# Kernel tuning notes

Hardware: AMD Instinct MI355X
Metric: run time of the kernel (lower is better)

Reference implementation:

```python
import jax, jax.numpy as jnp
import numpy as np

HIDDEN = 1024
NUM_HEADS = 16
HEAD_DIM = HIDDEN // NUM_HEADS


def setup_inputs() -> dict:
    key = jax.random.key(0)
    k1, k2, k3, k4, k5 = jax.random.split(key, 5)
    B, S, T, H = 2, 2048, 2048, HIDDEN
    scale = 0.02
    return {
        "query": jax.random.normal(k1, (B, S, H), dtype=jnp.float32),
        "key_value": jax.random.normal(k2, (B, T, H), dtype=jnp.float32),
        "Wq": jax.random.normal(k3, (H, H), dtype=jnp.float32) * scale,
        "Wkv": jax.random.normal(k4, (H, 2 * H), dtype=jnp.float32) * scale,
        "Wc": jax.random.normal(k5, (H, H), dtype=jnp.float32) * scale,
    }


def reference(query, key_value, Wq, Wkv, Wc):
    B, S, H = query.shape
    T = key_value.shape[1]
    nh, hd = NUM_HEADS, HEAD_DIM

    q = query @ Wq                                  # [B,S,H]
    kv = key_value @ Wkv                            # [B,T,2H]
    k, v = kv[..., :H], kv[..., H:]

    # [B, nh, S|T, hd]
    q = q.reshape(B, S, nh, hd).transpose(0, 2, 1, 3)
    k = k.reshape(B, T, nh, hd).transpose(0, 2, 1, 3)
    v = v.reshape(B, T, nh, hd).transpose(0, 2, 1, 3)

    scale = hd ** -0.5
    scores = jnp.einsum("bhsd,bhtd->bhst", q * scale, k)   # [B,nh,S,T]
    probs = jax.nn.softmax(scores, axis=-1)
    y = jnp.einsum("bhst,bhtd->bhsd", probs, v)             # [B,nh,S,hd]
    y = y.transpose(0, 2, 1, 3).reshape(B, S, H)
    return y @ Wc
```

## Files before the change

### kernel.cpp

```cpp
#include <hip/hip_runtime.h>
#include <hip/hip_bf16.h>


typedef unsigned short u16;
typedef __attribute__((ext_vector_type(4))) float float4v;
typedef __attribute__((ext_vector_type(4))) unsigned short u16x4;
typedef __attribute__((ext_vector_type(8))) short short8;
typedef __attribute__((ext_vector_type(4))) float floatx4;

__device__ __forceinline__ u16 f2bf(float f) {
  unsigned u = __float_as_uint(f);
  u += 0x7fffu + ((u >> 16) & 1u);
  return (u16)(u >> 16);
}

__device__ __forceinline__ float fast_exp2(float x) {
#if __has_builtin(__builtin_amdgcn_exp2f)
  return __builtin_amdgcn_exp2f(x);
#else
  return exp2f(x);
#endif
}

__device__ __forceinline__ unsigned pack_bf2(float a, float b) {
#if __has_builtin(__builtin_amdgcn_cvt_pk_bf16_f32)
  auto r = __builtin_amdgcn_cvt_pk_bf16_f32(a, b);
  unsigned u;
  __builtin_memcpy(&u, &r, 4);
  return u;
#else
  unsigned ua = __float_as_uint(a) + 0x7fffu + ((__float_as_uint(a) >> 16) & 1u);
  unsigned ub = __float_as_uint(b) + 0x7fffu + ((__float_as_uint(b) >> 16) & 1u);
  return __builtin_amdgcn_perm(ub, ua, 0x07060302u);
#endif
}

__device__ __forceinline__ void gld16(const void* g, void* l) {
  __builtin_amdgcn_global_load_lds(
      (const __attribute__((address_space(1))) void*)g,
      (__attribute__((address_space(3))) void*)l, 16, 0, 0);
}

#define WBAR(N) asm volatile("s_waitcnt vmcnt(" #N ") lgkmcnt(0)\n\ts_barrier" ::: "memory")

__device__ __forceinline__ int swz4(int r) { return (r & 3) ^ ((r >> 2) & 3); }

__global__ void prep(const float* __restrict__ X, const float* __restrict__ KV,
                     const float* __restrict__ Wq, const float* __restrict__ Wkv,
                     const float* __restrict__ Wc,
                     u16* __restrict__ qin, u16* __restrict__ kvin,
                     u16* __restrict__ Wqt, u16* __restrict__ Wkvt,
                     u16* __restrict__ Wct) {
  __shared__ float tile[32][33];
  const int bid = blockIdx.x, t = threadIdx.x;
  if (bid < 8192) {
    const float* src = bid < 4096 ? X : KV;
    u16* dst = bid < 4096 ? qin : kvin;
    int i = (bid & 4095) * 256 + t;
    float4v v = ((const float4v*)src)[i];
    u16x4 o;
    o.x = f2bf(v.x); o.y = f2bf(v.y); o.z = f2bf(v.z); o.w = f2bf(v.w);
    ((u16x4*)dst)[i] = o;
  } else {
    int r = bid - 8192;
    const float* in;
    u16* out;
    int C, bx, by;
    if (r < 1024)      { in = Wq;  out = Wqt;  C = 1024; bx = r & 31; by = r >> 5; }
    else if (r < 3072) { r -= 1024; in = Wkv; out = Wkvt; C = 2048; bx = r & 63; by = r >> 6; }
    else               { r -= 3072; in = Wc;  out = Wct;  C = 1024; bx = r & 31; by = r >> 5; }
    const int tx = t & 31, ty = t >> 5;
#pragma unroll
    for (int i = 0; i < 32; i += 8)
      tile[ty + i][tx] = in[(size_t)(by * 32 + ty + i) * C + bx * 32 + tx];
    __syncthreads();
#pragma unroll
    for (int i = 0; i < 32; i += 8)
      out[(size_t)(bx * 32 + ty + i) * 1024 + by * 32 + tx] = f2bf(tile[tx][ty + i]);
  }
}

__global__ __launch_bounds__(256, 3) void gemm_qkv(const u16* __restrict__ qin,
                                                   const u16* __restrict__ kvin,
                                                   const u16* __restrict__ Wqt,
                                                   const u16* __restrict__ Wkvt,
                                                   u16* __restrict__ qp,
                                                   u16* __restrict__ kp,
                                                   u16* __restrict__ vt,
                                                   float qscale) {
  __shared__ __align__(16) u16 Shm[24576];
  u16* As = Shm;
  u16* Bs = Shm + 12288;
  const int t = threadIdx.x;
  const int w = t >> 6, l = t & 63;
  const int lane15 = l & 15, quad = l >> 4;
  const int wm = w >> 1, wn = w & 1;

  const int bid = blockIdx.x;
  const int xr = bid & 7, g = bid >> 3;
  const int bx = 12 * (xr & 1) + g % 12;
  const int by = 8 * (xr >> 1) + g / 12;
  const int bm = by * 128;

  const int mode = bx >> 3;
  const u16* A = (mode == 0) ? qin : kvin;
  const u16* Bt = (mode == 0) ? Wqt : Wkvt;
  const int bn = (mode == 2) ? 1024 + (bx - 16) * 128 : (bx & 7) * 128;

  const int srow = t >> 2;
  const int scol = (((t & 3) ^ swz4(srow)) << 3);
  const u16* ag0 = A + (size_t)(bm + srow) * 1024 + scol;
  const u16* ag1 = ag0 + (size_t)64 * 1024;
  const u16* bg0 = Bt + (size_t)(bn + srow) * 1024 + scol;
  const u16* bg1 = bg0 + (size_t)64 * 1024;

  int afo[4], bfo[4];
#pragma unroll
  for (int mi = 0; mi < 4; ++mi) {
    int row = wm * 64 + mi * 16 + lane15;
    afo[mi] = row * 32 + ((quad ^ swz4(row)) << 3);
  }
#pragma unroll
  for (int ni = 0; ni < 4; ++ni) {
    int row = wn * 64 + ni * 16 + lane15;
    bfo[ni] = row * 32 + ((quad ^ swz4(row)) << 3);
  }

  floatx4 acc[4][4] = {};
  const bool vswap = (mode == 2);

  auto stage = [&](int kt, int buf) {
    gld16(ag0 + kt, &As[buf * 4096 + t * 8]);
    gld16(ag1 + kt, &As[buf * 4096 + 2048 + t * 8]);
    gld16(bg0 + kt, &Bs[buf * 4096 + t * 8]);
    gld16(bg1 + kt, &Bs[buf * 4096 + 2048 + t * 8]);
  };
  auto compute = [&](int buf) {
    short8 af[4], bf[4];
#pragma unroll
    for (int mi = 0; mi < 4; ++mi) af[mi] = *(const short8*)&As[buf * 4096 + afo[mi]];
#pragma unroll
    for (int ni = 0; ni < 4; ++ni) bf[ni] = *(const short8*)&Bs[buf * 4096 + bfo[ni]];
    if (!vswap) {
#pragma unroll
      for (int mi = 0; mi < 4; ++mi)
#pragma unroll
        for (int ni = 0; ni < 4; ++ni)
          acc[mi][ni] = __builtin_amdgcn_mfma_f32_16x16x32_bf16(af[mi], bf[ni],
                                                                acc[mi][ni], 0, 0, 0);
    } else {
#pragma unroll
      for (int mi = 0; mi < 4; ++mi)
#pragma unroll
        for (int ni = 0; ni < 4; ++ni)
          acc[mi][ni] = __builtin_amdgcn_mfma_f32_16x16x32_bf16(bf[ni], af[mi],
                                                                acc[mi][ni], 0, 0, 0);
    }
  };

  stage(0, 0);
  stage(32, 1);
#pragma unroll
  for (int it = 0; it < 30; ++it) {
    WBAR(4);
    compute(it % 3);
    stage((it + 2) * 32, (it + 2) % 3);
  }
  WBAR(4);
  compute(0);
  WBAR(0);
  compute(1);

  const float scale = (mode == 0) ? qscale : 1.0f;
  __syncthreads();
#pragma unroll
  for (int mi = 0; mi < 4; ++mi)
#pragma unroll
    for (int ni = 0; ni < 4; ++ni)
#pragma unroll
      for (int r = 0; r < 4; ++r) {
        int rl, cl;
        if (!vswap) {
          rl = wm * 64 + mi * 16 + quad * 4 + r;
          cl = wn * 64 + ni * 16 + lane15;
        } else {
          rl = wn * 64 + ni * 16 + quad * 4 + r;
          cl = wm * 64 + mi * 16 + lane15;
        }
        Shm[rl * 128 + (cl ^ ((rl & 3) << 4))] = f2bf(acc[mi][ni][r] * scale);
      }
  __syncthreads();
#pragma unroll
  for (int j = 0; j < 8; ++j) {
    int c = t + j * 256;
    int row = c >> 4, ch = c & 15;
    short8 v = *(const short8*)&Shm[row * 128 + ((ch ^ ((row & 3) << 1)) << 3)];
    if (mode == 0)
      *(short8*)&qp[(size_t)(bm + row) * 1024 + bn + ch * 8] = v;
    else if (mode == 1)
      *(short8*)&kp[(size_t)(bm + row) * 1024 + bn + ch * 8] = v;
    else {
      int b = bm >> 11;
      *(short8*)&vt[(size_t)(b * 1024 + (bn - 1024) + row) * 2048 +
                    (bm & 2047) + ch * 8] = v;
    }
  }
}

__global__ __launch_bounds__(256, 4) void gemm_out(const u16* __restrict__ A,
                                                   const u16* __restrict__ Bt,
                                                   float* __restrict__ C) {
  __shared__ __align__(16) u16 Shm[18432];
  u16* As = Shm;
  u16* Bs = Shm + 12288;
  float* Shf = (float*)Shm;
  const int t = threadIdx.x;
  const int w = t >> 6, l = t & 63;
  const int lane15 = l & 15, quad = l >> 4;
  const int wm = w >> 1, wn = w & 1;

  const int bid = blockIdx.x;
  const int xr = bid & 7, g = bid >> 3;
  const int bx = 8 * (xr & 1) + g % 8;
  const int by = 8 * (xr >> 1) + g / 8;
  const int bm = by * 128, bn = bx * 64;

  const int srow = t >> 2;
  const int scol = (((t & 3) ^ swz4(srow)) << 3);
  const u16* ag0 = A + (size_t)(bm + srow) * 1024 + scol;
  const u16* ag1 = ag0 + (size_t)64 * 1024;
  const u16* bg0 = Bt + (size_t)(bn + srow) * 1024 + scol;

  int afo[4], bfo[2];
#pragma unroll
  for (int mi = 0; mi < 4; ++mi) {
    int row = wm * 64 + mi * 16 + lane15;
    afo[mi] = row * 32 + ((quad ^ swz4(row)) << 3);
  }
#pragma unroll
  for (int ni = 0; ni < 2; ++ni) {
    int row = wn * 32 + ni * 16 + lane15;
    bfo[ni] = row * 32 + ((quad ^ swz4(row)) << 3);
  }

  floatx4 acc[4][2] = {};

  auto stage = [&](int kt, int buf) {
    gld16(ag0 + kt, &As[buf * 4096 + t * 8]);
    gld16(ag1 + kt, &As[buf * 4096 + 2048 + t * 8]);
    gld16(bg0 + kt, &Bs[buf * 2048 + t * 8]);
  };
  auto compute = [&](int buf) {
    short8 af[4], bf[2];
#pragma unroll
    for (int mi = 0; mi < 4; ++mi) af[mi] = *(const short8*)&As[buf * 4096 + afo[mi]];
#pragma unroll
    for (int ni = 0; ni < 2; ++ni) bf[ni] = *(const short8*)&Bs[buf * 2048 + bfo[ni]];
#pragma unroll
    for (int mi = 0; mi < 4; ++mi)
#pragma unroll
      for (int ni = 0; ni < 2; ++ni)
        acc[mi][ni] = __builtin_amdgcn_mfma_f32_16x16x32_bf16(af[mi], bf[ni],
                                                              acc[mi][ni], 0, 0, 0);
  };

  stage(0, 0);
  stage(32, 1);
#pragma unroll
  for (int it = 0; it < 30; ++it) {
    WBAR(3);
    compute(it % 3);
    stage((it + 2) * 32, (it + 2) % 3);
  }
  WBAR(3);
  compute(0);
  WBAR(0);
  compute(1);

  __syncthreads();
#pragma unroll
  for (int mi = 0; mi < 4; ++mi)
#pragma unroll
    for (int ni = 0; ni < 2; ++ni)
#pragma unroll
      for (int r = 0; r < 4; ++r) {
        int rl = wm * 64 + mi * 16 + quad * 4 + r;
        int cl = wn * 32 + ni * 16 + lane15;
        Shf[rl * 64 + (cl ^ ((rl & 3) << 4))] = acc[mi][ni][r];
      }
  __syncthreads();
#pragma unroll
  for (int j = 0; j < 8; ++j) {
    int c = t + j * 256;
    int row = c >> 4, ch = c & 15;
    float4v v = *(const float4v*)&Shf[row * 64 + ((ch ^ ((row & 3) << 2)) << 2)];
    *(float4v*)&C[(size_t)(bm + row) * 1024 + bn + ch * 4] = v;
  }
}

__global__ __launch_bounds__(512) void attn_kern(const u16* __restrict__ Q,
                                                 const u16* __restrict__ KP,
                                                 const u16* __restrict__ VT,
                                                 u16* __restrict__ Y) {
  __shared__ __align__(16) u16 Ks[3 * 4096];
  __shared__ __align__(16) u16 VTs[3 * 4096];
  __shared__ __align__(16) u16 Ps[8192];
  const int t = threadIdx.x, w = t >> 6, l = t & 63;
  const int lane15 = l & 15, quad = l >> 4;

  const int bid = blockIdx.x;
  const int xr = bid & 7, g = bid >> 3;
  const int bxt = 8 * (xr & 1) + g % 8;
  const int bh = 8 * (xr >> 1) + g / 8;
  const int b = bh >> 4, h = bh & 15;
  const int qrow0 = b * 2048 + bxt * 128;
  const int xm = lane15 & 7;

  short8 qf[2];
#pragma unroll
  for (int ks = 0; ks < 2; ++ks)
    qf[ks] = *(const short8*)&Q[(size_t)(qrow0 + w * 16 + lane15) * 1024 +
                                h * 64 + ks * 32 + quad * 8];

  const short8 vones = {0x3F80, 0x3F80, 0x3F80, 0x3F80,
                        0x3F80, 0x3F80, 0x3F80, 0x3F80};

  floatx4 yacc[4] = {};
  floatx4 lacc = {};

  const int srow = t >> 3;
  const int scol = (((t & 7) ^ (srow & 7)) << 3);
  const u16* kg = KP + (size_t)(b * 2048 + srow) * 1024 + h * 64 + scol;
  const u16* vg = VT + (size_t)(bh * 64 + srow) * 2048 + scol;

  const int prow = (w * 16 + lane15) * 64;
  int kfo[2][4], vfo[2][4], pwo[4], pro[2];
#pragma unroll
  for (int ks = 0; ks < 2; ++ks)
#pragma unroll
    for (int ti = 0; ti < 4; ++ti)
      kfo[ks][ti] = (ti * 16 + lane15) * 64 + (((ks * 4 + quad) ^ xm) << 3);
#pragma unroll
  for (int ts = 0; ts < 2; ++ts) {
#pragma unroll
    for (int ni = 0; ni < 4; ++ni)
      vfo[ts][ni] = (ni * 16 + lane15) * 64 + (((ts * 4 + quad) ^ xm) << 3);
    pro[ts] = prow + (((ts * 4 + quad) ^ xm) << 3);
  }
#pragma unroll
  for (int ti = 0; ti < 4; ++ti)
    pwo[ti] = prow + (((ti * 2 + (quad >> 1)) ^ xm) << 3) + ((quad & 1) << 2);

  auto stage = [&](int t0n, int buf) {
    gld16(kg + (size_t)t0n * 1024, &Ks[buf * 4096 + t * 8]);
    gld16(vg + t0n, &VTs[buf * 4096 + t * 8]);
  };
  auto compute = [&](int buf) {
    floatx4 sacc[4] = {};
#pragma unroll
    for (int ks = 0; ks < 2; ++ks)
#pragma unroll
      for (int ti = 0; ti < 4; ++ti) {
        short8 kf = *(const short8*)&Ks[buf * 4096 + kfo[ks][ti]];
        sacc[ti] = __builtin_amdgcn_mfma_f32_16x16x32_bf16(kf, qf[ks], sacc[ti], 0, 0, 0);
      }
#pragma unroll
    for (int ti = 0; ti < 4; ++ti) {
      float p0 = fast_exp2(sacc[ti][0]);
      float p1 = fast_exp2(sacc[ti][1]);
      float p2 = fast_exp2(sacc[ti][2]);
      float p3 = fast_exp2(sacc[ti][3]);
      uint2 pk;
      pk.x = pack_bf2(p0, p1);
      pk.y = pack_bf2(p2, p3);
      *(uint2*)&Ps[pwo[ti]] = pk;
    }
#pragma unroll
    for (int ts = 0; ts < 2; ++ts) {
      short8 pf = *(const short8*)&Ps[pro[ts]];
      lacc = __builtin_amdgcn_mfma_f32_16x16x32_bf16(pf, vones, lacc, 0, 0, 0);
#pragma unroll
      for (int ni = 0; ni < 4; ++ni) {
        short8 vf = *(const short8*)&VTs[buf * 4096 + vfo[ts][ni]];
        yacc[ni] = __builtin_amdgcn_mfma_f32_16x16x32_bf16(pf, vf, yacc[ni], 0, 0, 0);
      }
    }
  };

  stage(0, 0);
  stage(64, 1);
  for (int i = 0; i < 10; ++i) {
    const int base = i * 192;
    WBAR(2);
    compute(0);
    stage(base + 128, 2);
    WBAR(2);
    compute(1);
    stage(base + 192, 0);
    WBAR(2);
    compute(2);
    stage(base + 256, 1);
  }
  WBAR(2);
  compute(0);
  WBAR(0);
  compute(1);

#pragma unroll
  for (int r = 0; r < 4; ++r) {
    float linv = 1.0f / lacc[r];
    int row = qrow0 + w * 16 + quad * 4 + r;
#pragma unroll
    for (int ni = 0; ni < 4; ++ni)
      Y[(size_t)row * 1024 + h * 64 + ni * 16 + lane15] = f2bf(yacc[ni][r] * linv);
  }
}

extern "C" void kernel_launch(void* const* d_in, const int* in_sizes, int n_in,
                              void* d_out, int out_size, void* d_ws, size_t ws_size,
                              hipStream_t stream) {
  const float* query = (const float*)d_in[0];
  const float* key_value = (const float*)d_in[1];
  const float* Wq = (const float*)d_in[2];
  const float* Wkv = (const float*)d_in[3];
  const float* Wc = (const float*)d_in[4];
  float* out = (float*)d_out;

  const size_t MB = 1024 * 1024;
  char* ws = (char*)d_ws;
  u16* qin  = (u16*)(ws + 0 * MB);
  u16* kvin = (u16*)(ws + 8 * MB);
  u16* Wqt  = (u16*)(ws + 16 * MB);
  u16* Wkvt = (u16*)(ws + 18 * MB);
  u16* Wct  = (u16*)(ws + 22 * MB);
  u16* qp   = (u16*)(ws + 24 * MB);
  u16* kp   = (u16*)(ws + 32 * MB);
  u16* vt   = (u16*)(ws + 40 * MB);
  u16* y    = (u16*)(ws + 48 * MB);

  prep<<<dim3(12288), dim3(256), 0, stream>>>(query, key_value, Wq, Wkv, Wc,
                                              qin, kvin, Wqt, Wkvt, Wct);
  const float qscale = 0.125f * 1.4426950408889634f;
  gemm_qkv<<<dim3(768), dim3(256), 0, stream>>>(qin, kvin, Wqt, Wkvt,
                                                qp, kp, vt, qscale);
  attn_kern<<<dim3(512), dim3(512), 0, stream>>>(qp, kp, vt, y);
  gemm_out<<<dim3(512), dim3(256), 0, stream>>>(y, Wct, out);
}
```

Baseline: 187.5 us.

## Keep softmax probabilities in registers by permuting V^T token order

The P tile no longer round-trips through LDS. The exp'd score accumulators are packed directly into the MFMA A-operand registers. To make the register layout match the K dimension, the projection kernel writes V^T with a permuted token order inside each 64-token block (perm64), so the P·V contraction pairs the right elements. This removes an LDS write/read per tile and frees 16KB of shared memory. In exchange it couples the V layout to the attention fragment layout.

```diff
diff --git a/kernel.cpp b/kernel.cpp
--- a/kernel.cpp
+++ b/kernel.cpp
@@ -44,6 +44,10 @@
 #define WBAR(N) asm volatile("s_waitcnt vmcnt(" #N ") lgkmcnt(0)\n\ts_barrier" ::: "memory")
 
 __device__ __forceinline__ int swz4(int r) { return (r & 3) ^ ((r >> 2) & 3); }
+
+__device__ __forceinline__ int perm64(int x) {
+  return (x & 32) | ((x & 12) << 1) | ((x & 16) >> 2) | (x & 3);
+}
 
 __global__ void prep(const float* __restrict__ X, const float* __restrict__ KV,
                      const float* __restrict__ Wq, const float* __restrict__ Wkv,
@@ -185,7 +189,8 @@
           cl = wn * 64 + ni * 16 + lane15;
         } else {
           rl = wn * 64 + ni * 16 + quad * 4 + r;
-          cl = wm * 64 + mi * 16 + lane15;
+          int clr = wm * 64 + mi * 16 + lane15;
+          cl = (clr & 64) | perm64(clr & 63);
         }
         Shm[rl * 128 + (cl ^ ((rl & 3) << 4))] = f2bf(acc[mi][ni][r] * scale);
       }
@@ -304,7 +309,6 @@
                                                  u16* __restrict__ Y) {
   __shared__ __align__(16) u16 Ks[3 * 4096];
   __shared__ __align__(16) u16 VTs[3 * 4096];
-  __shared__ __align__(16) u16 Ps[8192];
   const int t = threadIdx.x, w = t >> 6, l = t & 63;
   const int lane15 = l & 15, quad = l >> 4;
 
@@ -333,23 +337,17 @@
   const u16* kg = KP + (size_t)(b * 2048 + srow) * 1024 + h * 64 + scol;
   const u16* vg = VT + (size_t)(bh * 64 + srow) * 2048 + scol;
 
-  const int prow = (w * 16 + lane15) * 64;
-  int kfo[2][4], vfo[2][4], pwo[4], pro[2];
+  int kfo[2][4], vfo[2][4];
 #pragma unroll
   for (int ks = 0; ks < 2; ++ks)
 #pragma unroll
     for (int ti = 0; ti < 4; ++ti)
       kfo[ks][ti] = (ti * 16 + lane15) * 64 + (((ks * 4 + quad) ^ xm) << 3);
 #pragma unroll
-  for (int ts = 0; ts < 2; ++ts) {
+  for (int ts = 0; ts < 2; ++ts)
 #pragma unroll
     for (int ni = 0; ni < 4; ++ni)
       vfo[ts][ni] = (ni * 16 + lane15) * 64 + (((ts * 4 + quad) ^ xm) << 3);
-    pro[ts] = prow + (((ts * 4 + quad) ^ xm) << 3);
-  }
-#pragma unroll
-  for (int ti = 0; ti < 4; ++ti)
-    pwo[ti] = prow + (((ti * 2 + (quad >> 1)) ^ xm) << 3) + ((quad & 1) << 2);
 
   auto stage = [&](int t0n, int buf) {
     gld16(kg + (size_t)t0n * 1024, &Ks[buf * 4096 + t * 8]);
@@ -364,25 +362,23 @@
         short8 kf = *(const short8*)&Ks[buf * 4096 + kfo[ks][ti]];
         sacc[ti] = __builtin_amdgcn_mfma_f32_16x16x32_bf16(kf, qf[ks], sacc[ti], 0, 0, 0);
       }
-#pragma unroll
-    for (int ti = 0; ti < 4; ++ti) {
-      float p0 = fast_exp2(sacc[ti][0]);
-      float p1 = fast_exp2(sacc[ti][1]);
-      float p2 = fast_exp2(sacc[ti][2]);
-      float p3 = fast_exp2(sacc[ti][3]);
-      uint2 pk;
-      pk.x = pack_bf2(p0, p1);
-      pk.y = pack_bf2(p2, p3);
-      *(uint2*)&Ps[pwo[ti]] = pk;
-    }
+    float p[4][4];
+#pragma unroll
+    for (int ti = 0; ti < 4; ++ti)
+#pragma unroll
+      for (int r = 0; r < 4; ++r) p[ti][r] = fast_exp2(sacc[ti][r]);
 #pragma unroll
     for (int ts = 0; ts < 2; ++ts) {
-      short8 pf = *(const short8*)&Ps[pro[ts]];
-      lacc = __builtin_amdgcn_mfma_f32_16x16x32_bf16(pf, vones, lacc, 0, 0, 0);
+      union { short8 s; unsigned u[4]; } pf;
+      pf.u[0] = pack_bf2(p[2 * ts][0], p[2 * ts][1]);
+      pf.u[1] = pack_bf2(p[2 * ts][2], p[2 * ts][3]);
+      pf.u[2] = pack_bf2(p[2 * ts + 1][0], p[2 * ts + 1][1]);
+      pf.u[3] = pack_bf2(p[2 * ts + 1][2], p[2 * ts + 1][3]);
+      lacc = __builtin_amdgcn_mfma_f32_16x16x32_bf16(pf.s, vones, lacc, 0, 0, 0);
 #pragma unroll
       for (int ni = 0; ni < 4; ++ni) {
         short8 vf = *(const short8*)&VTs[buf * 4096 + vfo[ts][ni]];
-        yacc[ni] = __builtin_amdgcn_mfma_f32_16x16x32_bf16(pf, vf, yacc[ni], 0, 0, 0);
+        yacc[ni] = __builtin_amdgcn_mfma_f32_16x16x32_bf16(pf.s, vf, yacc[ni], 0, 0, 0);
       }
     }
   };
```

Measured after the change: 182.5 us. -2.7%, faster.
